# Kernel optimization log

Measured on AMD Instinct MI355X. Metric: run time of the kernel, lower is better.

The kernel has to match this reference:

```python
import jax, jax.numpy as jnp
import numpy as np

B, S, P = 1024, 4096, 512


def setup_inputs() -> dict:
    key = jax.random.key(0)
    k1, k2 = jax.random.split(key, 2)
    idx = jax.random.randint(k1, (B, S), 0, P, dtype=jnp.int32)
    ds = jax.random.uniform(k2, (B, S), minval=1.0, maxval=20.0, dtype=jnp.float32)
    return {
        "idx": idx,
        "ds": ds,
        "sum_duration": jnp.zeros((P,), jnp.float32),
        "cnt_duration": jnp.zeros((P,), jnp.float32),
        "duration": jnp.zeros((P,), jnp.float32),
        "rv": jnp.full((1,), 0.5, jnp.float32),   # module hardcodes 0.5
        "dn": jnp.zeros((1,), jnp.float32),
        "padding_idx": 0,
    }


def reference(idx, ds, sum_duration, cnt_duration, duration, rv, dn, padding_idx):
    """Training-step scatter update of the running-average table, followed by the
    eval-branch gather + per-sequence duration rescaling (same math as the torch
    nested loops, fully vectorized)."""
    flat = idx.reshape(-1)
    # --- training branch: per-phone running average (scatter-add + divide) ---
    sum_new = sum_duration.at[flat].add(ds.reshape(-1))
    cnt_new = cnt_duration.at[flat].add(1.0)
    touched = jnp.zeros_like(duration).at[flat].add(1.0) > 0
    duration_new = jnp.where(touched, sum_new / jnp.maximum(cnt_new, 1.0), duration)
    has_26 = ((idx > 1) & (idx < 7)).any()
    dn_stat = sum_new[2:7].sum() / cnt_new[2:7].sum()
    dn_new = jnp.where(has_26, dn_stat, dn[0])  # scalar

    # --- eval branch: gather lookup + per-sequence rescaling ---
    # assignment of float duration into an int tensor truncates toward zero
    dur = jnp.trunc(duration_new)[idx].astype(jnp.int32)  # [B,S]
    seqlen = idx.shape[1]
    pad = idx[:, 1:] == padding_idx                        # [B,S-1]
    has_pad = pad.any(axis=1)
    first = jnp.argmax(pad, axis=1) + 1                    # first padding position >=1
    n = jnp.where(has_pad, first, 1)                       # [B]; n stays 1 if no pad
    j = jnp.arange(seqlen)[None, :]
    mid = (j >= 1) & (j < n[:, None])                      # positions 1..n-1
    denom = jnp.sum(jnp.where(mid, dur, 0), axis=1).astype(jnp.float32)
    dn_i = jnp.trunc(dn_new)
    num = dn_i - jnp.trunc(rv[0] * dn_new)                 # int(dn) - int(rv*dn)
    rc = jnp.where(n == 1, 1.0,
                   jnp.minimum(1.0, num / jnp.where(denom > 0, denom, 1.0)))  # [B]
    delta = jnp.maximum(dur[:, 1:].max(axis=1), 1)         # clamp delta >= 1
    dur0 = jnp.maximum(1, dn_i.astype(jnp.int32) - delta)  # [B]
    rescaled = jnp.maximum(
        1, jnp.trunc(rc[:, None] * dur.astype(jnp.float32)).astype(jnp.int32))
    dur_out = jnp.where(mid, rescaled, dur)
    dur_out = dur_out.at[:, 0].set(dur0)
    return dur_out, duration_new, dn_new
```

## Files before the change

### kernel.cpp

```cpp
#include <hip/hip_runtime.h>
#include <cstdint>

constexpr int B_ = 1024;
constexpr int S_ = 4096;
constexpr int P_ = 512;
constexpr int NSCAT = 512;

constexpr float FPSCALE = 2097152.0f;
constexpr double INV_FPSCALE = 1.0 / 2097152.0;

__global__ __launch_bounds__(256) void scatter_kernel(
    const int* __restrict__ idx, const float* __restrict__ ds,
    float* __restrict__ part) {
  __shared__ unsigned long long acc[4][P_];
  const int t = threadIdx.x;
  const int w = t >> 6;
#pragma unroll
  for (int c = 0; c < 4; ++c) {
    acc[c][t] = 0ull; acc[c][t + 256] = 0ull;
  }
  __syncthreads();

  unsigned long long* __restrict__ ma = acc[w];
  const size_t base = (size_t)blockIdx.x * 8192 + (size_t)t * 4;
#pragma unroll
  for (int k = 0; k < 8; k += 2) {
    const size_t off0 = base + (size_t)k * 1024;
    const size_t off1 = off0 + 1024;
    int4   i0 = *reinterpret_cast<const int4*>(idx + off0);
    int4   i1 = *reinterpret_cast<const int4*>(idx + off1);
    float4 d0 = *reinterpret_cast<const float4*>(ds + off0);
    float4 d1 = *reinterpret_cast<const float4*>(ds + off1);
    atomicAdd(&ma[i0.x], (1ull << 48) | (unsigned long long)(d0.x * FPSCALE));
    atomicAdd(&ma[i0.y], (1ull << 48) | (unsigned long long)(d0.y * FPSCALE));
    atomicAdd(&ma[i0.z], (1ull << 48) | (unsigned long long)(d0.z * FPSCALE));
    atomicAdd(&ma[i0.w], (1ull << 48) | (unsigned long long)(d0.w * FPSCALE));
    atomicAdd(&ma[i1.x], (1ull << 48) | (unsigned long long)(d1.x * FPSCALE));
    atomicAdd(&ma[i1.y], (1ull << 48) | (unsigned long long)(d1.y * FPSCALE));
    atomicAdd(&ma[i1.z], (1ull << 48) | (unsigned long long)(d1.z * FPSCALE));
    atomicAdd(&ma[i1.w], (1ull << 48) | (unsigned long long)(d1.w * FPSCALE));
  }
  __syncthreads();

  const int b0 = 2 * t, b1 = 2 * t + 1;
  const unsigned long long v0 =
      acc[0][b0] + acc[1][b0] + acc[2][b0] + acc[3][b0];
  const unsigned long long v1 =
      acc[0][b1] + acc[1][b1] + acc[2][b1] + acc[3][b1];
  const unsigned long long MASK48 = (1ull << 48) - 1;
  float4 ov;
  ov.x = (float)((double)(v0 & MASK48) * INV_FPSCALE);
  ov.y = (float)(v0 >> 48);
  ov.z = (float)((double)(v1 & MASK48) * INV_FPSCALE);
  ov.w = (float)(v1 >> 48);
  *reinterpret_cast<float4*>(part + (size_t)blockIdx.x * 1024 + 4 * t) = ov;
}

__global__ __launch_bounds__(256) void reduce_finalize_kernel(
    const float* __restrict__ part,
    const float* __restrict__ sum_in, const float* __restrict__ cnt_in,
    const float* __restrict__ dur_in,
    float* __restrict__ table, float* __restrict__ stats,
    float* __restrict__ out_tail ) {
  __shared__ float2 sred[256];
  const int t = threadIdx.x;
  const int p = blockIdx.x;

  const float2 a = *reinterpret_cast<const float2*>(
      part + (size_t)t * 1024 + 2 * p);
  const float2 b = *reinterpret_cast<const float2*>(
      part + (size_t)(t + 256) * 1024 + 2 * p);
  sred[t] = make_float2(a.x + b.x, a.y + b.y);
  __syncthreads();

  if (t < 128) {
    sred[t].x += sred[t + 128].x;
    sred[t].y += sred[t + 128].y;
  }
  __syncthreads();

  if (t < 64) {
    float ss = sred[t].x + sred[t + 64].x;
    float cc = sred[t].y + sred[t + 64].y;
#pragma unroll
    for (int o = 32; o > 0; o >>= 1) {
      ss += __shfl_down(ss, o);
      cc += __shfl_down(cc, o);
    }
    if (t == 0) {
      const float sn = ss + sum_in[p];
      const float cn = cc + cnt_in[p];
      const float tv = (cc > 0.f) ? sn / fmaxf(cn, 1.f) : dur_in[p];
      table[p]    = tv;
      out_tail[p] = tv;
      if (p >= 2 && p < 7) {
        stats[p - 2]      = sn;
        stats[5 + p - 2]  = cn;
        stats[10 + p - 2] = cc;
      }
    }
  }
}

__global__ __launch_bounds__(256) void eval_kernel(
    const int* __restrict__ idx, const float* __restrict__ table,
    const float* __restrict__ stats, const float* __restrict__ rv,
    const float* __restrict__ dn_in, const int* __restrict__ padp,
    float* __restrict__ out) {
  __shared__ float tbl[P_];
  __shared__ int   red_a[4], red_b[4], red_c[4];
  __shared__ int   bcast[3];
  __shared__ float fbcast[2];

  const int t   = threadIdx.x;
  const int row = blockIdx.x;
  tbl[t]       = table[t];
  tbl[t + 256] = table[t + 256];
  const int pad = padp[0];

  if (t == 0) {
    float ss = 0.f, cc = 0.f, rc = 0.f;
#pragma unroll
    for (int i = 0; i < 5; ++i) {
      ss += stats[i]; cc += stats[5 + i]; rc += stats[10 + i];
    }
    const float dnn = (rc > 0.f) ? (ss / cc) : dn_in[0];
    const float dni = truncf(dnn);
    fbcast[0] = dni;
    fbcast[1] = dni - truncf(rv[0] * dnn);
    if (row == 0) out[(size_t)B_ * S_ + P_] = dnn;
  }
  __syncthreads();

  const int* __restrict__ rowidx = idx + (size_t)row * S_;
  int d[16];
  int jfirst = 0x7fffffff;
  int dmax   = 0x80000000;

#pragma unroll
  for (int k = 0; k < 4; ++k) {
    const int j0 = k * 1024 + t * 4;
    int4 iv = *reinterpret_cast<const int4*>(rowidx + j0);
    const int ivm[4] = {iv.x, iv.y, iv.z, iv.w};
#pragma unroll
    for (int m = 0; m < 4; ++m) {
      const int j = j0 + m;
      const int dd = (int)tbl[ivm[m]];
      d[k * 4 + m] = dd;
      if (j >= 1) {
        if (ivm[m] == pad && j < jfirst) jfirst = j;
        if (dd > dmax) dmax = dd;
      }
    }
  }

  const int wid = t >> 6, lane = t & 63;
  int a = jfirst, b = dmax;
#pragma unroll
  for (int o = 32; o > 0; o >>= 1) {
    a = min(a, __shfl_down(a, o));
    b = max(b, __shfl_down(b, o));
  }
  if (lane == 0) { red_a[wid] = a; red_b[wid] = b; }
  __syncthreads();
  if (t == 0) {
    int na = min(min(red_a[0], red_a[1]), min(red_a[2], red_a[3]));
    int nb = max(max(red_b[0], red_b[1]), max(red_b[2], red_b[3]));
    bcast[0] = (na == 0x7fffffff) ? 1 : na;
    bcast[1] = nb;
  }
  __syncthreads();
  const int n       = bcast[0];
  const int dmaxall = bcast[1];

  int dsum = 0;
#pragma unroll
  for (int k = 0; k < 4; ++k) {
    const int j0 = k * 1024 + t * 4;
#pragma unroll
    for (int m = 0; m < 4; ++m) {
      const int j = j0 + m;
      if (j >= 1 && j < n) dsum += d[k * 4 + m];
    }
  }
#pragma unroll
  for (int o = 32; o > 0; o >>= 1) dsum += __shfl_down(dsum, o);
  if (lane == 0) red_c[wid] = dsum;
  __syncthreads();
  if (t == 0) bcast[2] = red_c[0] + red_c[1] + red_c[2] + red_c[3];
  __syncthreads();
  const int denom = bcast[2];

  const float dni = fbcast[0];
  const float num = fbcast[1];
  const float denomf = (float)denom;
  const float rc = (n == 1) ? 1.0f
                            : fminf(1.0f, num / (denomf > 0.f ? denomf : 1.0f));
  const int delta = max(dmaxall, 1);
  const int dur0  = max(1, (int)dni - delta);

  float* __restrict__ rowout = out + (size_t)row * S_;
#pragma unroll
  for (int k = 0; k < 4; ++k) {
    const int j0 = k * 1024 + t * 4;
    float4 ov;
    float* o = reinterpret_cast<float*>(&ov);
#pragma unroll
    for (int m = 0; m < 4; ++m) {
      const int j = j0 + m;
      const int dd = d[k * 4 + m];
      int v;
      if (j == 0)      v = dur0;
      else if (j < n)  v = max(1, (int)truncf(rc * (float)dd));
      else             v = dd;
      o[m] = (float)v;
    }
    *reinterpret_cast<float4*>(rowout + j0) = ov;
  }
}

extern "C" void kernel_launch(void* const* d_in, const int* in_sizes, int n_in,
                              void* d_out, int out_size, void* d_ws, size_t ws_size,
                              hipStream_t stream) {
  const int*   idx    = (const int*)d_in[0];
  const float* ds     = (const float*)d_in[1];
  const float* sum_in = (const float*)d_in[2];
  const float* cnt_in = (const float*)d_in[3];
  const float* dur_in = (const float*)d_in[4];
  const float* rv     = (const float*)d_in[5];
  const float* dn     = (const float*)d_in[6];
  const int*   pad    = (const int*)d_in[7];

  float* out = (float*)d_out;

  float* part  = (float*)d_ws;
  float* table = part + (size_t)NSCAT * 1024;
  float* stats = table + P_;

  scatter_kernel<<<NSCAT, 256, 0, stream>>>(idx, ds, part);
  reduce_finalize_kernel<<<P_, 256, 0, stream>>>(part, sum_in, cnt_in, dur_in,
                                                 table, stats,
                                                 out + (size_t)B_ * S_);
  eval_kernel<<<1024, 256, 0, stream>>>(idx, table, stats, rv, dn, pad, out);
}
```

Baseline: 25.55 us.

## Replace partials+reduce kernel with global 64-bit atomics and fuse finalize into eval

Each scatter block now merges its shared-memory packed sum/count histogram into a global 64-bit accumulator with atomics, padded to 8-element stride to spread contention. This removes the partials buffer and the separate reduce kernel. Every eval block rebuilds the lookup table and dn statistics from the accumulator, and row 0 writes the duration table output. A memset launch is added, and the finalize arithmetic is now repeated in all 1024 eval blocks.

```diff
diff --git a/kernel.cpp b/kernel.cpp
--- a/kernel.cpp
+++ b/kernel.cpp
@@ -5,23 +5,24 @@
 constexpr int S_ = 4096;
 constexpr int P_ = 512;
 constexpr int NSCAT = 512;
+constexpr int ASTRIDE = 8;
 
 constexpr float FPSCALE = 2097152.0f;
 constexpr double INV_FPSCALE = 1.0 / 2097152.0;
 
 __global__ __launch_bounds__(256) void scatter_kernel(
     const int* __restrict__ idx, const float* __restrict__ ds,
-    float* __restrict__ part) {
-  __shared__ unsigned long long acc[4][P_];
+    unsigned long long* __restrict__ acc) {
+  __shared__ unsigned long long lacc[4][P_];
   const int t = threadIdx.x;
   const int w = t >> 6;
 #pragma unroll
   for (int c = 0; c < 4; ++c) {
-    acc[c][t] = 0ull; acc[c][t + 256] = 0ull;
-  }
-  __syncthreads();
-
-  unsigned long long* __restrict__ ma = acc[w];
+    lacc[c][t] = 0ull; lacc[c][t + 256] = 0ull;
+  }
+  __syncthreads();
+
+  unsigned long long* __restrict__ ma = lacc[w];
   const size_t base = (size_t)blockIdx.x * 8192 + (size_t)t * 4;
 #pragma unroll
   for (int k = 0; k < 8; k += 2) {
@@ -44,67 +45,17 @@
 
   const int b0 = 2 * t, b1 = 2 * t + 1;
   const unsigned long long v0 =
-      acc[0][b0] + acc[1][b0] + acc[2][b0] + acc[3][b0];
+      lacc[0][b0] + lacc[1][b0] + lacc[2][b0] + lacc[3][b0];
   const unsigned long long v1 =
-      acc[0][b1] + acc[1][b1] + acc[2][b1] + acc[3][b1];
-  const unsigned long long MASK48 = (1ull << 48) - 1;
-  float4 ov;
-  ov.x = (float)((double)(v0 & MASK48) * INV_FPSCALE);
-  ov.y = (float)(v0 >> 48);
-  ov.z = (float)((double)(v1 & MASK48) * INV_FPSCALE);
-  ov.w = (float)(v1 >> 48);
-  *reinterpret_cast<float4*>(part + (size_t)blockIdx.x * 1024 + 4 * t) = ov;
+      lacc[0][b1] + lacc[1][b1] + lacc[2][b1] + lacc[3][b1];
+  if (v0) atomicAdd(&acc[(size_t)b0 * ASTRIDE], v0);
+  if (v1) atomicAdd(&acc[(size_t)b1 * ASTRIDE], v1);
 }
 
-__global__ __launch_bounds__(256) void reduce_finalize_kernel(
-    const float* __restrict__ part,
+__global__ __launch_bounds__(256) void eval_kernel(
+    const int* __restrict__ idx, const unsigned long long* __restrict__ acc,
     const float* __restrict__ sum_in, const float* __restrict__ cnt_in,
-    const float* __restrict__ dur_in,
-    float* __restrict__ table, float* __restrict__ stats,
-    float* __restrict__ out_tail ) {
-  __shared__ float2 sred[256];
-  const int t = threadIdx.x;
-  const int p = blockIdx.x;
-
-  const float2 a = *reinterpret_cast<const float2*>(
-      part + (size_t)t * 1024 + 2 * p);
-  const float2 b = *reinterpret_cast<const float2*>(
-      part + (size_t)(t + 256) * 1024 + 2 * p);
-  sred[t] = make_float2(a.x + b.x, a.y + b.y);
-  __syncthreads();
-
-  if (t < 128) {
-    sred[t].x += sred[t + 128].x;
-    sred[t].y += sred[t + 128].y;
-  }
-  __syncthreads();
-
-  if (t < 64) {
-    float ss = sred[t].x + sred[t + 64].x;
-    float cc = sred[t].y + sred[t + 64].y;
-#pragma unroll
-    for (int o = 32; o > 0; o >>= 1) {
-      ss += __shfl_down(ss, o);
-      cc += __shfl_down(cc, o);
-    }
-    if (t == 0) {
-      const float sn = ss + sum_in[p];
-      const float cn = cc + cnt_in[p];
-      const float tv = (cc > 0.f) ? sn / fmaxf(cn, 1.f) : dur_in[p];
-      table[p]    = tv;
-      out_tail[p] = tv;
-      if (p >= 2 && p < 7) {
-        stats[p - 2]      = sn;
-        stats[5 + p - 2]  = cn;
-        stats[10 + p - 2] = cc;
-      }
-    }
-  }
-}
-
-__global__ __launch_bounds__(256) void eval_kernel(
-    const int* __restrict__ idx, const float* __restrict__ table,
-    const float* __restrict__ stats, const float* __restrict__ rv,
+    const float* __restrict__ dur_in, const float* __restrict__ rv,
     const float* __restrict__ dn_in, const int* __restrict__ padp,
     float* __restrict__ out) {
   __shared__ float tbl[P_];
@@ -114,15 +65,39 @@
 
   const int t   = threadIdx.x;
   const int row = blockIdx.x;
-  tbl[t]       = table[t];
-  tbl[t + 256] = table[t + 256];
   const int pad = padp[0];
+  const unsigned long long MASK48 = (1ull << 48) - 1;
+
+  {
+    const unsigned long long v0 = acc[(size_t)t * ASTRIDE];
+    const unsigned long long v1 = acc[(size_t)(t + 256) * ASTRIDE];
+    const float c0 = (float)(v0 >> 48);
+    const float c1 = (float)(v1 >> 48);
+    const float s0 = (float)((double)(v0 & MASK48) * INV_FPSCALE);
+    const float s1 = (float)((double)(v1 & MASK48) * INV_FPSCALE);
+    const float sn0 = s0 + sum_in[t];
+    const float sn1 = s1 + sum_in[t + 256];
+    const float cn0 = c0 + cnt_in[t];
+    const float cn1 = c1 + cnt_in[t + 256];
+    const float tv0 = (c0 > 0.f) ? sn0 / fmaxf(cn0, 1.f) : dur_in[t];
+    const float tv1 = (c1 > 0.f) ? sn1 / fmaxf(cn1, 1.f) : dur_in[t + 256];
+    tbl[t]       = tv0;
+    tbl[t + 256] = tv1;
+    if (row == 0) {
+      out[(size_t)B_ * S_ + t]       = tv0;
+      out[(size_t)B_ * S_ + t + 256] = tv1;
+    }
+  }
 
   if (t == 0) {
     float ss = 0.f, cc = 0.f, rc = 0.f;
 #pragma unroll
-    for (int i = 0; i < 5; ++i) {
-      ss += stats[i]; cc += stats[5 + i]; rc += stats[10 + i];
+    for (int i = 2; i < 7; ++i) {
+      const unsigned long long v = acc[(size_t)i * ASTRIDE];
+      const float craw = (float)(v >> 48);
+      ss += (float)((double)(v & MASK48) * INV_FPSCALE) + sum_in[i];
+      cc += craw + cnt_in[i];
+      rc += craw;
     }
     const float dnn = (rc > 0.f) ? (ss / cc) : dn_in[0];
     const float dni = truncf(dnn);
@@ -232,14 +207,11 @@
   const int*   pad    = (const int*)d_in[7];
 
   float* out = (float*)d_out;
-
-  float* part  = (float*)d_ws;
-  float* table = part + (size_t)NSCAT * 1024;
-  float* stats = table + P_;
-
-  scatter_kernel<<<NSCAT, 256, 0, stream>>>(idx, ds, part);
-  reduce_finalize_kernel<<<P_, 256, 0, stream>>>(part, sum_in, cnt_in, dur_in,
-                                                 table, stats,
-                                                 out + (size_t)B_ * S_);
-  eval_kernel<<<1024, 256, 0, stream>>>(idx, table, stats, rv, dn, pad, out);
+  unsigned long long* acc = (unsigned long long*)d_ws;
+
+  hipMemsetAsync(acc, 0, (size_t)P_ * ASTRIDE * sizeof(unsigned long long),
+                 stream);
+  scatter_kernel<<<NSCAT, 256, 0, stream>>>(idx, ds, acc);
+  eval_kernel<<<B_, 256, 0, stream>>>(idx, acc, sum_in, cnt_in, dur_in,
+                                      rv, dn, pad, out);
 }
```

After: 36.11 us. +41.4%, slower.
